# Performance work log

Measured on AMD Instinct MI355X. Metric: run time of the kernel, lower is better.

## Reference

```python
import jax, jax.numpy as jnp
import numpy as np

TEMPERATURE = 0.07
EPS = 1e-12


def setup_inputs() -> dict:
    key = jax.random.key(0)
    k1, k2 = jax.random.split(key)
    B, D = 16384, 256
    return {
        "query_embeds": jax.random.normal(k1, (B, D), dtype=jnp.float32),
        "database_embeds": jax.random.normal(k2, (B, D), dtype=jnp.float32),
    }


def _l2_normalize(x, axis=1):
    # torch F.normalize: x / max(||x||, eps)
    norm = jnp.sqrt(jnp.sum(x * x, axis=axis, keepdims=True))
    return x / jnp.maximum(norm, EPS)


def reference(query_embeds, database_embeds):
    q = _l2_normalize(query_embeds, axis=1)   # [B, D]
    d = _l2_normalize(database_embeds, axis=1)  # [B, D]
    sim = jnp.einsum("bd,cd->bc", q, d) / TEMPERATURE  # [B, B]
    B = sim.shape[0]
    diag = jnp.diagonal(sim)  # logits at the correct (matching) label
    # CE over rows (q->d): -log_softmax(sim, axis=1)[i, i]
    lse_rows = jax.nn.logsumexp(sim, axis=1)
    loss_q2d = jnp.mean(lse_rows - diag)
    # CE over rows of sim.T == columns of sim (d->q)
    lse_cols = jax.nn.logsumexp(sim, axis=0)
    loss_d2q = jnp.mean(lse_cols - diag)
    return (loss_q2d + loss_d2q) / 2
```

## Files before the change

kernel.cpp:

```cpp
#include <hip/hip_runtime.h>
#include <hip/hip_bf16.h>
#include <cstdint>
#include <cstddef>

#define B_ROWS 16384
#define D_DIM  256
#define TEMP_INV 14.285714285714286f

#define BM 128
#define BN 128
#define BK 128

using frag_cd = __attribute__((ext_vector_type(4))) float;
using i32x4   = __attribute__((ext_vector_type(4))) int;
using i32x8   = __attribute__((ext_vector_type(8))) int;

__device__ __forceinline__ void gld_lds16(const void* g, void* l) {
    __builtin_amdgcn_global_load_lds(
        (const __attribute__((address_space(1))) void*)g,
        (__attribute__((address_space(3))) void*)l,
        16, 0, 0);
}

__global__ __launch_bounds__(256) void norm_diag_kernel(
    const float* __restrict__ q, const float* __restrict__ d,
    unsigned int* __restrict__ qn, unsigned int* __restrict__ dn,
    float* __restrict__ diag,
    float* __restrict__ row_sums, float* __restrict__ col_sums,
    float* __restrict__ out) {
    const int b = blockIdx.x;
    if (b < 64)            row_sums[b * 256 + threadIdx.x] = 0.0f;
    else if (b < 128)      col_sums[(b - 64) * 256 + threadIdx.x] = 0.0f;
    else if (b == 128 && threadIdx.x == 0) out[0] = 0.0f;

    const int row  = b * 4 + (threadIdx.x >> 6);
    const int lane = threadIdx.x & 63;

    const float4 qv = ((const float4*)(q + (size_t)row * D_DIM))[lane];
    const float4 dv = ((const float4*)(d + (size_t)row * D_DIM))[lane];

    float qss = qv.x*qv.x + qv.y*qv.y + qv.z*qv.z + qv.w*qv.w;
    float dss = dv.x*dv.x + dv.y*dv.y + dv.z*dv.z + dv.w*dv.w;
    float qd  = qv.x*dv.x + qv.y*dv.y + qv.z*dv.z + qv.w*dv.w;
#pragma unroll
    for (int off = 32; off; off >>= 1) {
        qss += __shfl_down(qss, off);
        dss += __shfl_down(dss, off);
        qd  += __shfl_down(qd,  off);
    }
    qss = __shfl(qss, 0);
    dss = __shfl(dss, 0);
    qd  = __shfl(qd,  0);

    const float qinv = 1.0f / fmaxf(sqrtf(qss), 1e-12f);
    const float dinv = 1.0f / fmaxf(sqrtf(dss), 1e-12f);

    int qp = 0, dp = 0;
    qp = __builtin_amdgcn_cvt_pk_fp8_f32(qv.x * qinv, qv.y * qinv, qp, false);
    qp = __builtin_amdgcn_cvt_pk_fp8_f32(qv.z * qinv, qv.w * qinv, qp, true);
    dp = __builtin_amdgcn_cvt_pk_fp8_f32(dv.x * dinv, dv.y * dinv, dp, false);
    dp = __builtin_amdgcn_cvt_pk_fp8_f32(dv.z * dinv, dv.w * dinv, dp, true);
    qn[row * (D_DIM / 4) + lane] = (unsigned int)qp;
    dn[row * (D_DIM / 4) + lane] = (unsigned int)dp;

    if (lane == 0) diag[row] = qd * qinv * dinv * TEMP_INV;
}

__global__ __launch_bounds__(256, 4) void gemm_lse_kernel(
    const unsigned char* __restrict__ qn, const unsigned char* __restrict__ dn,
    float* __restrict__ row_sums, float* __restrict__ col_sums) {
    __shared__ unsigned char As[BM][BK];
    __shared__ unsigned char Bs[BN][BK];

    const int t    = threadIdx.x;
    const int lane = t & 63;
    const int w    = t >> 6;
    const int l15  = lane & 15;
    const int quad = lane >> 4;
    const int m0   = (w >> 1) * 64;
    const int n0   = (w & 1) * 64;

    const int id  = blockIdx.x;
    const int xcd = id & 7;
    const int j   = id >> 3;
    const int bx  = (xcd << 4) | (j & 15);
    const int by  = j >> 4;
    const int rowBase = by * BM;
    const int colBase = bx * BN;

    const int rsub = t >> 3;
    const int g    = ((t & 7) ^ (rsub & 7)) << 4;
    const unsigned char* ga = qn + (size_t)(rowBase + rsub) * D_DIM + g;
    const unsigned char* gb = dn + (size_t)(colBase + rsub) * D_DIM + g;
    unsigned char* la = &As[0][0] + t * 16;
    unsigned char* lb = &Bs[0][0] + t * 16;

    frag_cd acc[4][4];
#pragma unroll
    for (int i = 0; i < 4; ++i)
#pragma unroll
        for (int jj = 0; jj < 4; ++jj)
            acc[i][jj] = (frag_cd){0.0f, 0.0f, 0.0f, 0.0f};

    const int PCa = quad ^ (l15 & 7);

    union OpU { i32x8 v; i32x4 h[2]; };

    for (int kt = 0; kt < D_DIM; kt += BK) {
        if (kt) __syncthreads();
#pragma unroll
        for (int it = 0; it < 4; ++it) {
            gld_lds16(ga + (size_t)it * 32 * D_DIM + kt, la + it * 32 * BK);
            gld_lds16(gb + (size_t)it * 32 * D_DIM + kt, lb + it * 32 * BK);
        }
        __syncthreads();

        OpU b8[4];
#pragma unroll
        for (int i = 0; i < 4; ++i) {
            const unsigned char* rB = &Bs[n0 + i * 16 + l15][0];
            b8[i].h[0] = *(const i32x4*)(rB + PCa * 16);
            b8[i].h[1] = *(const i32x4*)(rB + (PCa ^ 4) * 16);
        }
#pragma unroll
        for (int mi = 0; mi < 4; ++mi) {
            OpU a8;
            const unsigned char* rA = &As[m0 + mi * 16 + l15][0];
            a8.h[0] = *(const i32x4*)(rA + PCa * 16);
            a8.h[1] = *(const i32x4*)(rA + (PCa ^ 4) * 16);
#pragma unroll
            for (int ni = 0; ni < 4; ++ni)
                acc[mi][ni] = __builtin_amdgcn_mfma_scale_f32_16x16x128_f8f6f4(
                    a8.v, b8[ni].v, acc[mi][ni],
                    0, 0,
                    0, 0x7F7F7F7F,
                    0, 0x7F7F7F7F);
        }
    }

    const float C2 = TEMP_INV * 1.44269504088896f;
    union { frag_cd v[4]; float f[16]; } rvu;
    frag_cd cv4[4];
#pragma unroll
    for (int i = 0; i < 4; ++i) {
        rvu.v[i] = (frag_cd){0.0f, 0.0f, 0.0f, 0.0f};
        cv4[i]   = (frag_cd){0.0f, 0.0f, 0.0f, 0.0f};
    }
#pragma unroll
    for (int mi = 0; mi < 4; ++mi)
#pragma unroll
        for (int ni = 0; ni < 4; ++ni) {
            const frag_cd tt = acc[mi][ni] * C2 - C2;
            frag_cd e;
#pragma unroll
            for (int r = 0; r < 4; ++r) e[r] = __builtin_amdgcn_exp2f(tt[r]);
            rvu.v[mi] += e;
            cv4[ni]   += e;
        }
    float cv[4];
#pragma unroll
    for (int ni = 0; ni < 4; ++ni)
        cv[ni] = (cv4[ni][0] + cv4[ni][1]) + (cv4[ni][2] + cv4[ni][3]);

#pragma unroll
    for (int s = 0; s < 4; ++s) {
        const bool b = (l15 >> s) & 1;
#pragma unroll
        for (int i = 0; i < (8 >> s); ++i) {
            const float a0 = rvu.f[2 * i], a1 = rvu.f[2 * i + 1];
            const float keep = b ? a1 : a0;
            const float send = b ? a0 : a1;
            rvu.f[i] = keep + __shfl_xor(send, 1 << s);
        }
    }
    atomicAdd(&row_sums[rowBase + m0 + (l15 >> 2) * 16 + quad * 4 + (l15 & 3)], rvu.f[0]);

#pragma unroll
    for (int s = 0; s < 2; ++s) {
        const bool b = (quad >> s) & 1;
#pragma unroll
        for (int i = 0; i < (2 >> s); ++i) {
            const float a0 = cv[2 * i], a1 = cv[2 * i + 1];
            const float keep = b ? a1 : a0;
            const float send = b ? a0 : a1;
            cv[i] = keep + __shfl_xor(send, 16 << s);
        }
    }
    atomicAdd(&col_sums[colBase + n0 + quad * 16 + l15], cv[0]);
}

__global__ __launch_bounds__(256) void finalize_kernel(
    const float* __restrict__ rs, const float* __restrict__ cs,
    const float* __restrict__ dg, float* __restrict__ out) {
    const int i = blockIdx.x * 256 + threadIdx.x;
    float s = logf(rs[i]) + logf(cs[i]) - 2.0f * dg[i];
#pragma unroll
    for (int off = 32; off; off >>= 1) s += __shfl_down(s, off);
    __shared__ float buf[4];
    if ((threadIdx.x & 63) == 0) buf[threadIdx.x >> 6] = s;
    __syncthreads();
    if (threadIdx.x == 0) {
        float tot = (buf[0] + buf[1] + buf[2] + buf[3]) / (2.0f * B_ROWS);
        if (blockIdx.x == 0) tot += TEMP_INV;
        atomicAdd(out, tot);
    }
}

extern "C" void kernel_launch(void* const* d_in, const int* in_sizes, int n_in,
                              void* d_out, int out_size, void* d_ws, size_t ws_size,
                              hipStream_t stream) {
    const float* q = (const float*)d_in[0];
    const float* d = (const float*)d_in[1];
    float* out = (float*)d_out;

    char* ws = (char*)d_ws;
    unsigned char* qn = (unsigned char*)ws;
    unsigned char* dn = qn + (size_t)B_ROWS * D_DIM;
    float* row_sums = (float*)(ws + 2 * (size_t)B_ROWS * D_DIM);
    float* col_sums = row_sums + B_ROWS;
    float* diag     = col_sums + B_ROWS;

    norm_diag_kernel<<<B_ROWS / 4, 256, 0, stream>>>(
        q, d, (unsigned int*)qn, (unsigned int*)dn, diag, row_sums, col_sums, out);
    gemm_lse_kernel<<<(B_ROWS / BM) * (B_ROWS / BN), 256, 0, stream>>>(
        qn, dn, row_sums, col_sums);
    finalize_kernel<<<B_ROWS / 256, 256, 0, stream>>>(row_sums, col_sums, diag, out);
}
```

Baseline: 179.4 us.

## Store fp8 embeddings in MFMA fragment order and load operands directly from global

The normalize kernel now writes the fp8 embeddings in a tiled layout that matches the MFMA operand fragment order, so each lane's 16-byte chunk sits contiguously. The GEMM kernel then drops shared-memory staging and barriers and loads A/B fragments straight from global memory (L2/L1 cached). This removes LDS traffic and synchronization, but each wave reloads its operands independently, with more global/cache traffic and less latency hiding.

```diff
diff --git a/kernel.cpp b/kernel.cpp
--- a/kernel.cpp
+++ b/kernel.cpp
@@ -9,18 +9,11 @@
 
 #define BM 128
 #define BN 128
-#define BK 128
 
 using frag_cd = __attribute__((ext_vector_type(4))) float;
 using i32x4   = __attribute__((ext_vector_type(4))) int;
 using i32x8   = __attribute__((ext_vector_type(8))) int;
 
-__device__ __forceinline__ void gld_lds16(const void* g, void* l) {
-    __builtin_amdgcn_global_load_lds(
-        (const __attribute__((address_space(1))) void*)g,
-        (__attribute__((address_space(3))) void*)l,
-        16, 0, 0);
-}
 
 __global__ __launch_bounds__(256) void norm_diag_kernel(
     const float* __restrict__ q, const float* __restrict__ d,
@@ -60,8 +53,12 @@
     qp = __builtin_amdgcn_cvt_pk_fp8_f32(qv.z * qinv, qv.w * qinv, qp, true);
     dp = __builtin_amdgcn_cvt_pk_fp8_f32(dv.x * dinv, dv.y * dinv, dp, false);
     dp = __builtin_amdgcn_cvt_pk_fp8_f32(dv.z * dinv, dv.w * dinv, dp, true);
-    qn[row * (D_DIM / 4) + lane] = (unsigned int)qp;
-    dn[row * (D_DIM / 4) + lane] = (unsigned int)dp;
+
+    const int g = row >> 4;
+    const int widx = (g << 10) | ((lane >> 5) << 9) | (((lane >> 4) & 1) << 8)
+                   | (((lane >> 2) & 3) << 6) | ((row & 15) << 2) | (lane & 3);
+    qn[widx] = (unsigned int)qp;
+    dn[widx] = (unsigned int)dp;
 
     if (lane == 0) diag[row] = qd * qinv * dinv * TEMP_INV;
 }
@@ -69,9 +66,6 @@
 __global__ __launch_bounds__(256, 4) void gemm_lse_kernel(
     const unsigned char* __restrict__ qn, const unsigned char* __restrict__ dn,
     float* __restrict__ row_sums, float* __restrict__ col_sums) {
-    __shared__ unsigned char As[BM][BK];
-    __shared__ unsigned char Bs[BN][BK];
-
     const int t    = threadIdx.x;
     const int lane = t & 63;
     const int w    = t >> 6;
@@ -88,12 +82,8 @@
     const int rowBase = by * BM;
     const int colBase = bx * BN;
 
-    const int rsub = t >> 3;
-    const int g    = ((t & 7) ^ (rsub & 7)) << 4;
-    const unsigned char* ga = qn + (size_t)(rowBase + rsub) * D_DIM + g;
-    const unsigned char* gb = dn + (size_t)(colBase + rsub) * D_DIM + g;
-    unsigned char* la = &As[0][0] + t * 16;
-    unsigned char* lb = &Bs[0][0] + t * 16;
+    const unsigned char* aB = qn + ((size_t)((rowBase + m0) >> 4) << 12) + lane * 16;
+    const unsigned char* bB = dn + ((size_t)((colBase + n0) >> 4) << 12) + lane * 16;
 
     frag_cd acc[4][4];
 #pragma unroll
@@ -102,32 +92,21 @@
         for (int jj = 0; jj < 4; ++jj)
             acc[i][jj] = (frag_cd){0.0f, 0.0f, 0.0f, 0.0f};
 
-    const int PCa = quad ^ (l15 & 7);
-
     union OpU { i32x8 v; i32x4 h[2]; };
 
-    for (int kt = 0; kt < D_DIM; kt += BK) {
-        if (kt) __syncthreads();
-#pragma unroll
-        for (int it = 0; it < 4; ++it) {
-            gld_lds16(ga + (size_t)it * 32 * D_DIM + kt, la + it * 32 * BK);
-            gld_lds16(gb + (size_t)it * 32 * D_DIM + kt, lb + it * 32 * BK);
-        }
-        __syncthreads();
-
+#pragma unroll
+    for (int kt = 0; kt < 2; ++kt) {
         OpU b8[4];
 #pragma unroll
-        for (int i = 0; i < 4; ++i) {
-            const unsigned char* rB = &Bs[n0 + i * 16 + l15][0];
-            b8[i].h[0] = *(const i32x4*)(rB + PCa * 16);
-            b8[i].h[1] = *(const i32x4*)(rB + (PCa ^ 4) * 16);
+        for (int ni = 0; ni < 4; ++ni) {
+            b8[ni].h[0] = *(const i32x4*)(bB + (size_t)ni * 4096 + kt * 2048);
+            b8[ni].h[1] = *(const i32x4*)(bB + (size_t)ni * 4096 + kt * 2048 + 1024);
         }
 #pragma unroll
         for (int mi = 0; mi < 4; ++mi) {
             OpU a8;
-            const unsigned char* rA = &As[m0 + mi * 16 + l15][0];
-            a8.h[0] = *(const i32x4*)(rA + PCa * 16);
-            a8.h[1] = *(const i32x4*)(rA + (PCa ^ 4) * 16);
+            a8.h[0] = *(const i32x4*)(aB + (size_t)mi * 4096 + kt * 2048);
+            a8.h[1] = *(const i32x4*)(aB + (size_t)mi * 4096 + kt * 2048 + 1024);
 #pragma unroll
             for (int ni = 0; ni < 4; ++ni)
                 acc[mi][ni] = __builtin_amdgcn_mfma_scale_f32_16x16x128_f8f6f4(
```

New measurement: 204.6 us. 1.14x slower.
